# Kernel optimization log

Hardware: AMD Instinct MI355X
Metric: run time of the kernel (lower is better)

Reference implementation:

```python
import jax, jax.numpy as jnp
import numpy as np

NW = 30000      # num_words (word nodes)
ND = 8192       # num_docs
D = 300         # hidden_dim
D2 = D // 2
NNZ_A = 600000  # nnz of word-word adjacency A_norm [NW, NW]
NNZ_X = 524288  # nnz of doc-word tfidf X [ND, NW]
ALPHA = 0.7     # residual_alpha
LN_EPS = 1e-5
BN_SCALE = float(1.0 / np.sqrt(1.0 + 1e-5))  # eval BN, running_mean=0, running_var=1


def _xavier(k, shape):
    fan_out, fan_in = shape[0], shape[1]
    lim = float(np.sqrt(6.0 / (fan_in + fan_out)))
    return jax.random.uniform(k, shape, jnp.float32, -lim, lim)


def setup_inputs() -> dict:
    key = jax.random.key(0)
    ks = jax.random.split(key, 13)
    return {
        "a_rows": jax.random.randint(ks[0], (NNZ_A,), 0, NW, dtype=jnp.int32),
        "a_cols": jax.random.randint(ks[1], (NNZ_A,), 0, NW, dtype=jnp.int32),
        "a_vals": jax.random.uniform(ks[2], (NNZ_A,), jnp.float32) * 0.05,
        "x_rows": jax.random.randint(ks[3], (NNZ_X,), 0, ND, dtype=jnp.int32),
        "x_cols": jax.random.randint(ks[4], (NNZ_X,), 0, NW, dtype=jnp.int32),
        "x_vals": jax.random.uniform(ks[5], (NNZ_X,), jnp.float32) * 0.05,
        "emb": _xavier(ks[6], (NW, D)),
        "w1": _xavier(ks[7], (D, D)),
        "w2": _xavier(ks[8], (D, D)),
        "w3": _xavier(ks[9], (D, D)),
        "ln_g": jnp.ones((D,), jnp.float32),
        "ln_b": jnp.zeros((D,), jnp.float32),
        "m_w1": _xavier(ks[10], (D, D)),
        "m_b1": jnp.zeros((D,), jnp.float32),
        "bn1_g": jnp.ones((D,), jnp.float32),
        "bn1_b": jnp.zeros((D,), jnp.float32),
        "m_w2": _xavier(ks[11], (D2, D)),
        "m_b2": jnp.zeros((D2,), jnp.float32),
        "bn2_g": jnp.ones((D2,), jnp.float32),
        "bn2_b": jnp.zeros((D2,), jnp.float32),
        "clf_w": _xavier(ks[12], (2, D2)),
        "clf_b": jnp.zeros((2,), jnp.float32),
    }


def _spmm(rows, cols, vals, H, n):
    # sparse [n, m] @ dense [m, d] via gather + segment-sum (COO SpMM)
    return jax.ops.segment_sum(vals[:, None] * H[cols], rows, num_segments=n)


def _layernorm(x, g, b):
    mu = jnp.mean(x, axis=-1, keepdims=True)
    var = jnp.var(x, axis=-1, keepdims=True)
    return (x - mu) * jax.lax.rsqrt(var + LN_EPS) * g + b


def _bn_eval(x, g, b):
    # BatchNorm1d in eval mode with freshly-initialized running stats (mean=0, var=1)
    return x * (g * BN_SCALE) + b


def reference(a_rows, a_cols, a_vals, x_rows, x_cols, x_vals, emb, w1, w2, w3,
              ln_g, ln_b, m_w1, m_b1, bn1_g, bn1_b, m_w2, m_b2, bn2_g, bn2_b,
              clf_w, clf_b):
    H0 = emb
    H = jax.nn.relu(_spmm(a_rows, a_cols, a_vals, H0, NW) @ w1.T)
    H = jax.nn.relu(_spmm(a_rows, a_cols, a_vals, H, NW) @ w2.T)
    H = jax.nn.relu(_spmm(a_rows, a_cols, a_vals, H, NW) @ w3.T)
    H = (1.0 - ALPHA) * H0 + ALPHA * H
    word_H = _layernorm(H, ln_g, ln_b)
    # --- doc aggregation: X_tfidf @ word_H + X_tfidf @ emb ---
    doc_H = (_spmm(x_rows, x_cols, x_vals, word_H, ND)
             + _spmm(x_rows, x_cols, x_vals, emb, ND))
    # --- MLP head (dropout inactive in eval) ---
    h = jax.nn.relu(_bn_eval(doc_H @ m_w1.T + m_b1, bn1_g, bn1_b))
    h = jax.nn.relu(_bn_eval(h @ m_w2.T + m_b2, bn2_g, bn2_b))
    return h @ clf_w.T + clf_b  # [ND, 2]
```

## Files before the change

### kernel.cpp

```cpp
#include <hip/hip_runtime.h>

#define NW 30000
#define ND 8192
#define DIM 300
#define DIM2 150
#define NNZA 600000
#define NNZX 524288
#define PD 320
#define PD_U 160
#define BN_SCALE 0.99999500003749971f

typedef unsigned int uint;
typedef unsigned short ushort;
typedef __attribute__((ext_vector_type(8))) short bf16x8;
typedef __attribute__((ext_vector_type(4))) float f32x4;
typedef __attribute__((ext_vector_type(4))) uint uint4v;

static inline int cdiv(int a, int b){ return (a + b - 1) / b; }

__device__ __forceinline__ float b2f_lo(uint u){ return __builtin_bit_cast(float, u << 16); }
__device__ __forceinline__ float b2f_hi(uint u){ return __builtin_bit_cast(float, u & 0xffff0000u); }
__device__ __forceinline__ ushort f2b(float f){
  uint u = __builtin_bit_cast(uint, f);
  u += 0x7fffu + ((u >> 16) & 1u);
  return (ushort)(u >> 16);
}
__device__ __forceinline__ uint packb(float x, float y){
  return (uint)f2b(x) | ((uint)f2b(y) << 16);
}

__global__ void k_hist(const int* __restrict__ rows, int n, int* __restrict__ cnt){
  int i = blockIdx.x * blockDim.x + threadIdx.x;
  if (i < n) atomicAdd(&cnt[rows[i]], 1);
}

__global__ __launch_bounds__(1024) void k_bsum(const int* __restrict__ cnt, int n, int* __restrict__ bs){
  __shared__ int sd[1024];
  int t = threadIdx.x;
  int i = blockIdx.x * 1024 + t;
  sd[t] = (i < n) ? cnt[i] : 0;
  __syncthreads();
  #pragma unroll
  for (int o = 512; o > 0; o >>= 1){
    if (t < o) sd[t] += sd[t + o];
    __syncthreads();
  }
  if (t == 0) bs[blockIdx.x] = sd[0];
}

__global__ __launch_bounds__(64) void k_scan_small(int* __restrict__ bs, int nb,
                                                   int* __restrict__ rp, int n){
  int t = threadIdx.x;
  int orig = (t < nb) ? bs[t] : 0;
  int v = orig;
  #pragma unroll
  for (int o = 1; o < 64; o <<= 1){
    int x = __shfl_up(v, o);
    if (t >= o) v += x;
  }
  if (t < nb) bs[t] = v - orig;
  if (t == nb - 1) rp[n] = v;
}

__global__ __launch_bounds__(1024) void k_scan_apply(const int* __restrict__ cnt, int n,
        const int* __restrict__ bs, int* __restrict__ rp, int* __restrict__ cursor){
  __shared__ int sd[1024];
  int t = threadIdx.x;
  int i = blockIdx.x * 1024 + t;
  int v = (i < n) ? cnt[i] : 0;
  sd[t] = v;
  __syncthreads();
  for (int o = 1; o < 1024; o <<= 1){
    int x = (t >= o) ? sd[t - o] : 0;
    __syncthreads();
    sd[t] += x;
    __syncthreads();
  }
  if (i < n){
    int start = bs[blockIdx.x] + sd[t] - v;
    rp[i] = start;
    cursor[i] = start;
  }
}

__global__ void k_scatter(const int* __restrict__ rows, const int* __restrict__ cols,
                          const float* __restrict__ vals, int n, int* __restrict__ cursor,
                          int* __restrict__ cs, float* __restrict__ vs){
  int i = blockIdx.x * blockDim.x + threadIdx.x;
  if (i < n){
    int r = rows[i];
    int p = atomicAdd(&cursor[r], 1);
    cs[p] = cols[i];
    vs[p] = vals[i];
  }
}

__global__ void k_f2b_pad8(const float* __restrict__ src, ushort* __restrict__ dst,
                           int srows, int scols, int drows, int dstride){
  int q = blockIdx.x * blockDim.x + threadIdx.x;
  int perRow = dstride >> 3;
  int r = q / perRow;
  int c = (q - r * perRow) << 3;
  if (r >= drows) return;
  float x[8];
  #pragma unroll
  for (int j = 0; j < 8; ++j)
    x[j] = (r < srows && c + j < scols) ? src[(size_t)r * scols + c + j] : 0.f;
  uint4v o;
  o.x = packb(x[0], x[1]); o.y = packb(x[2], x[3]);
  o.z = packb(x[4], x[5]); o.w = packb(x[6], x[7]);
  *(uint4v*)(dst + (size_t)r * dstride + c) = o;
}

__global__ void k_f2b_w5(const float* __restrict__ w1, const float* __restrict__ w2,
                         const float* __restrict__ w3, const float* __restrict__ mw1,
                         const float* __restrict__ mw2,
                         ushort* __restrict__ d1, ushort* __restrict__ d2,
                         ushort* __restrict__ d3, ushort* __restrict__ d4,
                         ushort* __restrict__ d5){
  int q = blockIdx.x * blockDim.x + threadIdx.x;
  int r = q / 40;
  int c = (q - r * 40) << 3;
  if (r >= PD) return;
  const float* src; ushort* dst; int srows;
  int wsel = blockIdx.y;
  if      (wsel == 0){ src = w1;  dst = d1; srows = DIM;  }
  else if (wsel == 1){ src = w2;  dst = d2; srows = DIM;  }
  else if (wsel == 2){ src = w3;  dst = d3; srows = DIM;  }
  else if (wsel == 3){ src = mw1; dst = d4; srows = DIM;  }
  else               { src = mw2; dst = d5; srows = DIM2; }
  float x[8];
  #pragma unroll
  for (int j = 0; j < 8; ++j)
    x[j] = (r < srows && c + j < DIM) ? src[(size_t)r * DIM + c + j] : 0.f;
  uint4v o;
  o.x = packb(x[0], x[1]); o.y = packb(x[2], x[3]);
  o.z = packb(x[4], x[5]); o.w = packb(x[6], x[7]);
  *(uint4v*)(dst + (size_t)r * PD + c) = o;
}

__global__ __launch_bounds__(256) void k_spmm_b(const int* __restrict__ rp, const int* __restrict__ cs,
        const float* __restrict__ vs, const uint* __restrict__ Hb, uint* __restrict__ Ob, int nrows){
  int wid = (blockIdx.x * blockDim.x + threadIdx.x) >> 6;
  int lane = threadIdx.x & 63;
  if (wid >= nrows) return;
  int s = rp[wid], e = rp[wid + 1];
  const bool half = lane < 32;
  float acc[4][6] = {};
  int k = s;
  for (; k + 4 <= e; k += 4){
    #pragma unroll
    for (int j = 0; j < 4; ++j){
      int c = cs[k + j];
      float v = vs[k + j];
      const uint* p = Hb + (size_t)c * PD_U;
      uint u0 = p[lane], u1 = p[lane + 64];
      uint u2 = half ? p[lane + 128] : 0;
      acc[j][0] = fmaf(v, b2f_lo(u0), acc[j][0]);
      acc[j][1] = fmaf(v, b2f_hi(u0), acc[j][1]);
      acc[j][2] = fmaf(v, b2f_lo(u1), acc[j][2]);
      acc[j][3] = fmaf(v, b2f_hi(u1), acc[j][3]);
      acc[j][4] = fmaf(v, b2f_lo(u2), acc[j][4]);
      acc[j][5] = fmaf(v, b2f_hi(u2), acc[j][5]);
    }
  }
  for (; k < e; ++k){
    int c = cs[k];
    float v = vs[k];
    const uint* p = Hb + (size_t)c * PD_U;
    uint u0 = p[lane], u1 = p[lane + 64];
    uint u2 = half ? p[lane + 128] : 0;
    acc[0][0] = fmaf(v, b2f_lo(u0), acc[0][0]);
    acc[0][1] = fmaf(v, b2f_hi(u0), acc[0][1]);
    acc[0][2] = fmaf(v, b2f_lo(u1), acc[0][2]);
    acc[0][3] = fmaf(v, b2f_hi(u1), acc[0][3]);
    acc[0][4] = fmaf(v, b2f_lo(u2), acc[0][4]);
    acc[0][5] = fmaf(v, b2f_hi(u2), acc[0][5]);
  }
  #pragma unroll
  for (int d = 0; d < 6; ++d)
    acc[0][d] += (acc[1][d] + acc[2][d]) + acc[3][d];
  uint* o = Ob + (size_t)wid * PD_U;
  o[lane] = packb(acc[0][0], acc[0][1]);
  o[lane + 64] = packb(acc[0][2], acc[0][3]);
  if (half) o[lane + 128] = packb(acc[0][4], acc[0][5]);
}

__global__ __launch_bounds__(256) void k_mgemm(const ushort* __restrict__ A, const ushort* __restrict__ B,
        const float* __restrict__ bias, const float* __restrict__ bng, const float* __restrict__ bnb,
        ushort* __restrict__ C, int M, int Nvalid, int ldc, int relu){
  __shared__ ushort As[128][72];
  __shared__ ushort Bs[160][72];
  const int t = threadIdx.x;
  const int wid = t >> 6, lane = t & 63;
  const int bm = blockIdx.y << 7;
  const int bn = blockIdx.x * 160;
  const int wm = (wid >> 1) << 6;
  const int wn = (wid & 1) * 80;
  const int r16 = lane & 15;
  const int h8 = (lane >> 4) << 3;
  f32x4 acc[4][5] = {};
  for (int k0 = 0; k0 < PD; k0 += 64){
    #pragma unroll
    for (int i = 0; i < 4; ++i){
      int q = t + (i << 8);
      int r = q >> 3, c = (q & 7) << 3;
      int gm = bm + r; if (gm >= M) gm = M - 1;
      *(bf16x8*)(&As[r][c]) = *(const bf16x8*)(A + (size_t)gm * PD + k0 + c);
    }
    #pragma unroll
    for (int i = 0; i < 5; ++i){
      int q = t + (i << 8);
      int r = q >> 3, c = (q & 7) << 3;
      *(bf16x8*)(&Bs[r][c]) = *(const bf16x8*)(B + (size_t)(bn + r) * PD + k0 + c);
    }
    __syncthreads();
    #pragma unroll
    for (int kk = 0; kk < 2; ++kk){
      bf16x8 af[4], bfr[5];
      #pragma unroll
      for (int m = 0; m < 4; ++m)
        af[m] = *(const bf16x8*)(&As[wm + m * 16 + r16][kk * 32 + h8]);
      #pragma unroll
      for (int n = 0; n < 5; ++n)
        bfr[n] = *(const bf16x8*)(&Bs[wn + n * 16 + r16][kk * 32 + h8]);
      #pragma unroll
      for (int m = 0; m < 4; ++m)
        #pragma unroll
        for (int n = 0; n < 5; ++n)
          acc[m][n] = __builtin_amdgcn_mfma_f32_16x16x32_bf16(af[m], bfr[n], acc[m][n], 0, 0, 0);
    }
    __syncthreads();
  }
  const int cr = (lane >> 4) << 2;
  #pragma unroll
  for (int m = 0; m < 4; ++m){
    #pragma unroll
    for (int n = 0; n < 5; ++n){
      int col = bn + wn + n * 16 + r16;
      #pragma unroll
      for (int j = 0; j < 4; ++j){
        int row = bm + wm + m * 16 + cr + j;
        if (row >= M) continue;
        float v = acc[m][n][j];
        if (col < Nvalid){
          if (bias) v += bias[col];
          if (bng)  v = v * (bng[col] * BN_SCALE) + bnb[col];
          if (relu) v = fmaxf(v, 0.f);
        } else v = 0.f;
        C[(size_t)row * ldc + col] = f2b(v);
      }
    }
  }
}

__global__ __launch_bounds__(256) void k_res_ln(const float* __restrict__ emb, const uint* __restrict__ Hb,
        const float* __restrict__ g, const float* __restrict__ bb, uint* __restrict__ S){
  int row = blockIdx.x * 4 + (threadIdx.x >> 6);
  int lane = threadIdx.x & 63;
  if (row >= NW) return;
  const float* e = emb + (size_t)row * DIM;
  const uint* h = Hb + (size_t)row * PD_U;
  float x[6], ev[6];
  float sum = 0.f, sq = 0.f;
  #pragma unroll
  for (int j = 0; j < 3; ++j){
    int i = lane + j * 64;
    float e0 = 0.f, e1 = 0.f, h0 = 0.f, h1 = 0.f;
    if (i < 150){
      uint u = h[i];
      h0 = b2f_lo(u); h1 = b2f_hi(u);
      e0 = e[2 * i]; e1 = e[2 * i + 1];
    }
    float v0 = 0.3f * e0 + 0.7f * h0;
    float v1 = 0.3f * e1 + 0.7f * h1;
    if (i >= 150){ v0 = 0.f; v1 = 0.f; }
    x[2*j] = v0; x[2*j+1] = v1; ev[2*j] = e0; ev[2*j+1] = e1;
    sum += v0 + v1; sq += v0 * v0 + v1 * v1;
  }
  #pragma unroll
  for (int o = 32; o > 0; o >>= 1){ sum += __shfl_down(sum, o); sq += __shfl_down(sq, o); }
  sum = __shfl(sum, 0); sq = __shfl(sq, 0);
  const float inv = 1.f / (float)DIM;
  float mu = sum * inv;
  float var = sq * inv - mu * mu;
  float rs = rsqrtf(var + 1e-5f);
  uint* o = S + (size_t)row * PD_U;
  #pragma unroll
  for (int j = 0; j < 3; ++j){
    int i = lane + j * 64;
    if (i >= PD_U) continue;
    uint w = 0;
    if (i < 150){
      float r0 = (x[2*j]   - mu) * rs * g[2*i]   + bb[2*i]   + ev[2*j];
      float r1 = (x[2*j+1] - mu) * rs * g[2*i+1] + bb[2*i+1] + ev[2*j+1];
      w = packb(r0, r1);
    }
    o[i] = w;
  }
}

__global__ void k_clf(const uint* __restrict__ h2, const float* __restrict__ w,
                      const float* __restrict__ bias, float* __restrict__ out){
  int m = blockIdx.x * blockDim.x + threadIdx.x;
  if (m >= ND) return;
  const uint* hr = h2 + (size_t)m * 80;
  float s0 = bias[0], s1 = bias[1];
  #pragma unroll 5
  for (int i = 0; i < 75; ++i){
    uint u = hr[i];
    float h0 = b2f_lo(u), h1 = b2f_hi(u);
    int k = 2 * i;
    s0 = fmaf(h0, w[k], fmaf(h1, w[k + 1], s0));
    s1 = fmaf(h0, w[DIM2 + k], fmaf(h1, w[DIM2 + k + 1], s1));
  }
  out[m * 2] = s0;
  out[m * 2 + 1] = s1;
}

extern "C" void kernel_launch(void* const* d_in, const int* in_sizes, int n_in,
                              void* d_out, int out_size, void* d_ws, size_t ws_size,
                              hipStream_t stream){
  const int*   a_rows = (const int*)  d_in[0];
  const int*   a_cols = (const int*)  d_in[1];
  const float* a_vals = (const float*)d_in[2];
  const int*   x_rows = (const int*)  d_in[3];
  const int*   x_cols = (const int*)  d_in[4];
  const float* x_vals = (const float*)d_in[5];
  const float* emb    = (const float*)d_in[6];
  const float* w1     = (const float*)d_in[7];
  const float* w2     = (const float*)d_in[8];
  const float* w3     = (const float*)d_in[9];
  const float* ln_g   = (const float*)d_in[10];
  const float* ln_b   = (const float*)d_in[11];
  const float* m_w1   = (const float*)d_in[12];
  const float* m_b1   = (const float*)d_in[13];
  const float* bn1_g  = (const float*)d_in[14];
  const float* bn1_b  = (const float*)d_in[15];
  const float* m_w2   = (const float*)d_in[16];
  const float* m_b2   = (const float*)d_in[17];
  const float* bn2_g  = (const float*)d_in[18];
  const float* bn2_b  = (const float*)d_in[19];
  const float* clf_w  = (const float*)d_in[20];
  const float* clf_b  = (const float*)d_in[21];
  float* out = (float*)d_out;

  char* ws = (char*)d_ws;
  size_t off = 0;
  auto take = [&](size_t nbytes)->void*{
    void* p = ws + off;
    off += (nbytes + 255) & ~(size_t)255;
    return p;
  };
  int*    a_rp   = (int*)   take((NW + 1) * 4);
  int*    a_cs   = (int*)   take((size_t)NNZA * 4);
  float*  a_vs   = (float*) take((size_t)NNZA * 4);
  int*    x_rp   = (int*)   take((ND + 1) * 4);
  int*    x_cs   = (int*)   take((size_t)NNZX * 4);
  float*  x_vs   = (float*) take((size_t)NNZX * 4);
  int*    cursor = (int*)   take((size_t)NW * 4);
  int*    bsums  = (int*)   take(64 * 4);
  ushort* embb   = (ushort*)take((size_t)NW * PD * 2);
  ushort* Tb     = (ushort*)take((size_t)NW * PD * 2);
  ushort* Hb     = (ushort*)take((size_t)NW * PD * 2);
  ushort* w1b    = (ushort*)take((size_t)PD * PD * 2);
  ushort* w2b    = (ushort*)take((size_t)PD * PD * 2);
  ushort* w3b    = (ushort*)take((size_t)PD * PD * 2);
  ushort* mw1b   = (ushort*)take((size_t)PD * PD * 2);
  ushort* mw2b   = (ushort*)take((size_t)PD * PD * 2);
  ushort* docHb = Hb;
  ushort* h1b   = Hb + (size_t)ND * PD;
  ushort* h2b   = Hb + (size_t)2 * ND * PD;

  int nbA = cdiv(NW, 1024);
  hipMemsetAsync(cursor, 0, NW * 4, stream);
  k_hist<<<cdiv(NNZA, 256), 256, 0, stream>>>(a_rows, NNZA, cursor);
  k_bsum<<<nbA, 1024, 0, stream>>>(cursor, NW, bsums);
  k_scan_small<<<1, 64, 0, stream>>>(bsums, nbA, a_rp, NW);
  k_scan_apply<<<nbA, 1024, 0, stream>>>(cursor, NW, bsums, a_rp, cursor);
  k_scatter<<<cdiv(NNZA, 256), 256, 0, stream>>>(a_rows, a_cols, a_vals, NNZA, cursor, a_cs, a_vs);
  int nbX = cdiv(ND, 1024);
  hipMemsetAsync(cursor, 0, ND * 4, stream);
  k_hist<<<cdiv(NNZX, 256), 256, 0, stream>>>(x_rows, NNZX, cursor);
  k_bsum<<<nbX, 1024, 0, stream>>>(cursor, ND, bsums);
  k_scan_small<<<1, 64, 0, stream>>>(bsums, nbX, x_rp, ND);
  k_scan_apply<<<nbX, 1024, 0, stream>>>(cursor, ND, bsums, x_rp, cursor);
  k_scatter<<<cdiv(NNZX, 256), 256, 0, stream>>>(x_rows, x_cols, x_vals, NNZX, cursor, x_cs, x_vs);

  k_f2b_pad8<<<cdiv(NW * 40, 256), 256, 0, stream>>>(emb, embb, NW, DIM, NW, PD);
  dim3 gw(cdiv(PD * 40, 256), 5);
  k_f2b_w5<<<gw, 256, 0, stream>>>(w1, w2, w3, m_w1, m_w2, w1b, w2b, w3b, mw1b, mw2b);

  dim3 gg(2, cdiv(NW, 128));
  k_spmm_b<<<cdiv(NW, 4), 256, 0, stream>>>(a_rp, a_cs, a_vs, (const uint*)embb, (uint*)Tb, NW);
  k_mgemm<<<gg, 256, 0, stream>>>(Tb, w1b, nullptr, nullptr, nullptr, Hb, NW, DIM, PD, 1);
  k_spmm_b<<<cdiv(NW, 4), 256, 0, stream>>>(a_rp, a_cs, a_vs, (const uint*)Hb, (uint*)Tb, NW);
  k_mgemm<<<gg, 256, 0, stream>>>(Tb, w2b, nullptr, nullptr, nullptr, Hb, NW, DIM, PD, 1);
  k_spmm_b<<<cdiv(NW, 4), 256, 0, stream>>>(a_rp, a_cs, a_vs, (const uint*)Hb, (uint*)Tb, NW);
  k_mgemm<<<gg, 256, 0, stream>>>(Tb, w3b, nullptr, nullptr, nullptr, Hb, NW, DIM, PD, 1);
  k_res_ln<<<cdiv(NW, 4), 256, 0, stream>>>(emb, (const uint*)Hb, ln_g, ln_b, (uint*)Tb);
  k_spmm_b<<<cdiv(ND, 4), 256, 0, stream>>>(x_rp, x_cs, x_vs, (const uint*)Tb, (uint*)docHb, ND);
  dim3 g1(2, cdiv(ND, 128));
  k_mgemm<<<g1, 256, 0, stream>>>(docHb, mw1b, m_b1, bn1_g, bn1_b, h1b, ND, DIM, PD, 1);
  dim3 g2(1, cdiv(ND, 128));
  k_mgemm<<<g2, 256, 0, stream>>>(h1b, mw2b, m_b2, bn2_g, bn2_b, h2b, ND, DIM2, 160, 1);
  k_clf<<<cdiv(ND, 256), 256, 0, stream>>>((const uint*)h2b, clf_w, clf_b, out);
}
```

Baseline: 539.5 us.

## Merge CSR build and conversion launches, read bf16 emb in LN, warp-parallel classifier

Batches the A and X CSR construction (histogram, block sums, scan, scatter) and the emb/weight bf16 conversions into a few multi-purpose kernels selected by blockIdx.y. This cuts the launch count from about 14 to 5. The residual LayerNorm now reads the bf16-packed embedding instead of fp32 emb, which reduces its memory traffic but uses a rounded residual term. The classifier moves from one thread per row to one wavefront per row with shuffle reductions, for coalesced loads.

```diff
diff --git a/kernel.cpp b/kernel.cpp
--- a/kernel.cpp
+++ b/kernel.cpp
@@ -8,6 +8,8 @@
 #define NNZX 524288
 #define PD 320
 #define PD_U 160
+#define NBA 30
+#define NBX 8
 #define BN_SCALE 0.99999500003749971f
 
 typedef unsigned int uint;
@@ -29,13 +31,22 @@
   return (uint)f2b(x) | ((uint)f2b(y) << 16);
 }
 
-__global__ void k_hist(const int* __restrict__ rows, int n, int* __restrict__ cnt){
+__global__ void k_hist2(const int* __restrict__ ra, const int* __restrict__ rx,
+                        int* __restrict__ cntA, int* __restrict__ cntX){
   int i = blockIdx.x * blockDim.x + threadIdx.x;
-  if (i < n) atomicAdd(&cnt[rows[i]], 1);
-}
-
-__global__ __launch_bounds__(1024) void k_bsum(const int* __restrict__ cnt, int n, int* __restrict__ bs){
+  if (blockIdx.y == 0){
+    if (i < NNZA) atomicAdd(&cntA[ra[i]], 1);
+  } else {
+    if (i < NNZX) atomicAdd(&cntX[rx[i]], 1);
+  }
+}
+
+__global__ __launch_bounds__(1024) void k_bsum2(const int* __restrict__ cntA, const int* __restrict__ cntX,
+                                                int* __restrict__ bsA, int* __restrict__ bsX){
   __shared__ int sd[1024];
+  const int* cnt; int n; int* bs;
+  if (blockIdx.y == 0){ cnt = cntA; n = NW; bs = bsA; }
+  else                { cnt = cntX; n = ND; bs = bsX; }
   int t = threadIdx.x;
   int i = blockIdx.x * 1024 + t;
   sd[t] = (i < n) ? cnt[i] : 0;
@@ -48,23 +59,32 @@
   if (t == 0) bs[blockIdx.x] = sd[0];
 }
 
-__global__ __launch_bounds__(64) void k_scan_small(int* __restrict__ bs, int nb,
-                                                   int* __restrict__ rp, int n){
-  int t = threadIdx.x;
-  int orig = (t < nb) ? bs[t] : 0;
+__global__ __launch_bounds__(128) void k_scan_small2(int* __restrict__ bsA, int* __restrict__ bsX,
+                                                     int* __restrict__ a_rp, int* __restrict__ x_rp){
+  int w = threadIdx.x >> 6, lane = threadIdx.x & 63;
+  int* bs = w ? bsX : bsA;
+  int nb  = w ? NBX : NBA;
+  int* rp = w ? x_rp : a_rp;
+  int n   = w ? ND : NW;
+  int orig = (lane < nb) ? bs[lane] : 0;
   int v = orig;
   #pragma unroll
   for (int o = 1; o < 64; o <<= 1){
     int x = __shfl_up(v, o);
-    if (t >= o) v += x;
-  }
-  if (t < nb) bs[t] = v - orig;
-  if (t == nb - 1) rp[n] = v;
-}
-
-__global__ __launch_bounds__(1024) void k_scan_apply(const int* __restrict__ cnt, int n,
-        const int* __restrict__ bs, int* __restrict__ rp, int* __restrict__ cursor){
+    if (lane >= o) v += x;
+  }
+  if (lane < nb) bs[lane] = v - orig;
+  if (lane == nb - 1) rp[n] = v;
+}
+
+__global__ __launch_bounds__(1024) void k_scan_apply2(const int* __restrict__ cntA, const int* __restrict__ cntX,
+        const int* __restrict__ bsA, const int* __restrict__ bsX,
+        int* __restrict__ a_rp, int* __restrict__ x_rp,
+        int* __restrict__ curA, int* __restrict__ curX){
   __shared__ int sd[1024];
+  const int* cnt; const int* bs; int n; int* rp; int* cur;
+  if (blockIdx.y == 0){ cnt = cntA; bs = bsA; n = NW; rp = a_rp; cur = curA; }
+  else                { cnt = cntX; bs = bsX; n = ND; rp = x_rp; cur = curX; }
   int t = threadIdx.x;
   int i = blockIdx.x * 1024 + t;
   int v = (i < n) ? cnt[i] : 0;
@@ -79,64 +99,69 @@
   if (i < n){
     int start = bs[blockIdx.x] + sd[t] - v;
     rp[i] = start;
-    cursor[i] = start;
-  }
-}
-
-__global__ void k_scatter(const int* __restrict__ rows, const int* __restrict__ cols,
-                          const float* __restrict__ vals, int n, int* __restrict__ cursor,
-                          int* __restrict__ cs, float* __restrict__ vs){
-  int i = blockIdx.x * blockDim.x + threadIdx.x;
-  if (i < n){
-    int r = rows[i];
-    int p = atomicAdd(&cursor[r], 1);
-    cs[p] = cols[i];
-    vs[p] = vals[i];
-  }
-}
-
-__global__ void k_f2b_pad8(const float* __restrict__ src, ushort* __restrict__ dst,
-                           int srows, int scols, int drows, int dstride){
-  int q = blockIdx.x * blockDim.x + threadIdx.x;
-  int perRow = dstride >> 3;
-  int r = q / perRow;
-  int c = (q - r * perRow) << 3;
-  if (r >= drows) return;
-  float x[8];
-  #pragma unroll
-  for (int j = 0; j < 8; ++j)
-    x[j] = (r < srows && c + j < scols) ? src[(size_t)r * scols + c + j] : 0.f;
-  uint4v o;
-  o.x = packb(x[0], x[1]); o.y = packb(x[2], x[3]);
-  o.z = packb(x[4], x[5]); o.w = packb(x[6], x[7]);
-  *(uint4v*)(dst + (size_t)r * dstride + c) = o;
-}
-
-__global__ void k_f2b_w5(const float* __restrict__ w1, const float* __restrict__ w2,
-                         const float* __restrict__ w3, const float* __restrict__ mw1,
-                         const float* __restrict__ mw2,
-                         ushort* __restrict__ d1, ushort* __restrict__ d2,
-                         ushort* __restrict__ d3, ushort* __restrict__ d4,
-                         ushort* __restrict__ d5){
-  int q = blockIdx.x * blockDim.x + threadIdx.x;
-  int r = q / 40;
-  int c = (q - r * 40) << 3;
-  if (r >= PD) return;
-  const float* src; ushort* dst; int srows;
-  int wsel = blockIdx.y;
-  if      (wsel == 0){ src = w1;  dst = d1; srows = DIM;  }
-  else if (wsel == 1){ src = w2;  dst = d2; srows = DIM;  }
-  else if (wsel == 2){ src = w3;  dst = d3; srows = DIM;  }
-  else if (wsel == 3){ src = mw1; dst = d4; srows = DIM;  }
-  else               { src = mw2; dst = d5; srows = DIM2; }
-  float x[8];
-  #pragma unroll
-  for (int j = 0; j < 8; ++j)
-    x[j] = (r < srows && c + j < DIM) ? src[(size_t)r * DIM + c + j] : 0.f;
-  uint4v o;
-  o.x = packb(x[0], x[1]); o.y = packb(x[2], x[3]);
-  o.z = packb(x[4], x[5]); o.w = packb(x[6], x[7]);
-  *(uint4v*)(dst + (size_t)r * PD + c) = o;
+    cur[i] = start;
+  }
+}
+
+__global__ void k_prep(const int* __restrict__ a_rows, const int* __restrict__ a_cols, const float* __restrict__ a_vals,
+                       const int* __restrict__ x_rows, const int* __restrict__ x_cols, const float* __restrict__ x_vals,
+                       int* __restrict__ curA, int* __restrict__ curX,
+                       int* __restrict__ a_cs, float* __restrict__ a_vs,
+                       int* __restrict__ x_cs, float* __restrict__ x_vs,
+                       const float* __restrict__ emb, ushort* __restrict__ embb,
+                       const float* __restrict__ w1, const float* __restrict__ w2, const float* __restrict__ w3,
+                       const float* __restrict__ mw1, const float* __restrict__ mw2,
+                       ushort* __restrict__ w1b, ushort* __restrict__ w2b, ushort* __restrict__ w3b,
+                       ushort* __restrict__ mw1b, ushort* __restrict__ mw2b){
+  int y = blockIdx.y;
+  int gi = blockIdx.x * blockDim.x + threadIdx.x;
+  if (y == 0){
+    if (gi < NNZA){
+      int r = a_rows[gi];
+      int p = atomicAdd(&curA[r], 1);
+      a_cs[p] = a_cols[gi];
+      a_vs[p] = a_vals[gi];
+    }
+  } else if (y == 1){
+    if (gi < NNZX){
+      int r = x_rows[gi];
+      int p = atomicAdd(&curX[r], 1);
+      x_cs[p] = x_cols[gi];
+      x_vs[p] = x_vals[gi];
+    }
+  } else if (y == 2){
+    if (gi < NW * 40){
+      int r = gi / 40;
+      int c = (gi - r * 40) << 3;
+      float x[8];
+      #pragma unroll
+      for (int j = 0; j < 8; ++j)
+        x[j] = (c + j < DIM) ? emb[(size_t)r * DIM + c + j] : 0.f;
+      uint4v o;
+      o.x = packb(x[0], x[1]); o.y = packb(x[2], x[3]);
+      o.z = packb(x[4], x[5]); o.w = packb(x[6], x[7]);
+      *(uint4v*)(embb + (size_t)r * PD + c) = o;
+    }
+  } else {
+    if (gi < PD * 40){
+      int r = gi / 40;
+      int c = (gi - r * 40) << 3;
+      const float* src; ushort* dst; int srows;
+      if      (y == 3){ src = w1;  dst = w1b;  srows = DIM;  }
+      else if (y == 4){ src = w2;  dst = w2b;  srows = DIM;  }
+      else if (y == 5){ src = w3;  dst = w3b;  srows = DIM;  }
+      else if (y == 6){ src = mw1; dst = mw1b; srows = DIM;  }
+      else            { src = mw2; dst = mw2b; srows = DIM2; }
+      float x[8];
+      #pragma unroll
+      for (int j = 0; j < 8; ++j)
+        x[j] = (r < srows && c + j < DIM) ? src[(size_t)r * DIM + c + j] : 0.f;
+      uint4v o;
+      o.x = packb(x[0], x[1]); o.y = packb(x[2], x[3]);
+      o.z = packb(x[4], x[5]); o.w = packb(x[6], x[7]);
+      *(uint4v*)(dst + (size_t)r * PD + c) = o;
+    }
+  }
 }
 
 __global__ __launch_bounds__(256) void k_spmm_b(const int* __restrict__ rp, const int* __restrict__ cs,
@@ -254,12 +279,12 @@
   }
 }
 
-__global__ __launch_bounds__(256) void k_res_ln(const float* __restrict__ emb, const uint* __restrict__ Hb,
+__global__ __launch_bounds__(256) void k_res_ln(const uint* __restrict__ E, const uint* __restrict__ Hb,
         const float* __restrict__ g, const float* __restrict__ bb, uint* __restrict__ S){
   int row = blockIdx.x * 4 + (threadIdx.x >> 6);
   int lane = threadIdx.x & 63;
   if (row >= NW) return;
-  const float* e = emb + (size_t)row * DIM;
+  const uint* e = E + (size_t)row * PD_U;
   const uint* h = Hb + (size_t)row * PD_U;
   float x[6], ev[6];
   float sum = 0.f, sq = 0.f;
@@ -269,8 +294,9 @@
     float e0 = 0.f, e1 = 0.f, h0 = 0.f, h1 = 0.f;
     if (i < 150){
       uint u = h[i];
-      h0 = b2f_lo(u); h1 = b2f_hi(u);
-      e0 = e[2 * i]; e1 = e[2 * i + 1];
+      uint ue = e[i];
+      h0 = b2f_lo(u);  h1 = b2f_hi(u);
+      e0 = b2f_lo(ue); e1 = b2f_hi(ue);
     }
     float v0 = 0.3f * e0 + 0.7f * h0;
     float v1 = 0.3f * e1 + 0.7f * h1;
@@ -300,22 +326,35 @@
   }
 }
 
-__global__ void k_clf(const uint* __restrict__ h2, const float* __restrict__ w,
+__global__ __launch_bounds__(256) void k_clf(const uint* __restrict__ h2, const float* __restrict__ w,
                       const float* __restrict__ bias, float* __restrict__ out){
-  int m = blockIdx.x * blockDim.x + threadIdx.x;
-  if (m >= ND) return;
-  const uint* hr = h2 + (size_t)m * 80;
-  float s0 = bias[0], s1 = bias[1];
-  #pragma unroll 5
-  for (int i = 0; i < 75; ++i){
-    uint u = hr[i];
+  int row = blockIdx.x * 4 + (threadIdx.x >> 6);
+  int lane = threadIdx.x & 63;
+  if (row >= ND) return;
+  float s0, s1;
+  {
+    uint u = h2[(size_t)row * 80 + lane];
     float h0 = b2f_lo(u), h1 = b2f_hi(u);
-    int k = 2 * i;
-    s0 = fmaf(h0, w[k], fmaf(h1, w[k + 1], s0));
-    s1 = fmaf(h0, w[DIM2 + k], fmaf(h1, w[DIM2 + k + 1], s1));
-  }
-  out[m * 2] = s0;
-  out[m * 2 + 1] = s1;
+    int k = 2 * lane;
+    s0 = h0 * w[k] + h1 * w[k + 1];
+    s1 = h0 * w[DIM2 + k] + h1 * w[DIM2 + k + 1];
+  }
+  if (lane < 11){
+    uint u = h2[(size_t)row * 80 + 64 + lane];
+    float h0 = b2f_lo(u), h1 = b2f_hi(u);
+    int k = 2 * (64 + lane);
+    s0 += h0 * w[k] + h1 * w[k + 1];
+    s1 += h0 * w[DIM2 + k] + h1 * w[DIM2 + k + 1];
+  }
+  #pragma unroll
+  for (int o = 32; o > 0; o >>= 1){
+    s0 += __shfl_down(s0, o);
+    s1 += __shfl_down(s1, o);
+  }
+  if (lane == 0){
+    out[row * 2]     = s0 + bias[0];
+    out[row * 2 + 1] = s1 + bias[1];
+  }
 }
 
 extern "C" void kernel_launch(void* const* d_in, const int* in_sizes, int n_in,
@@ -358,8 +397,9 @@
   int*    x_rp   = (int*)   take((ND + 1) * 4);
   int*    x_cs   = (int*)   take((size_t)NNZX * 4);
   float*  x_vs   = (float*) take((size_t)NNZX * 4);
-  int*    cursor = (int*)   take((size_t)NW * 4);
-  int*    bsums  = (int*)   take(64 * 4);
+  int*    cursors= (int*)   take((size_t)(NW + ND) * 4);
+  int*    bsA    = (int*)   take(64 * 4);
+  int*    bsX    = (int*)   take(64 * 4);
   ushort* embb   = (ushort*)take((size_t)NW * PD * 2);
   ushort* Tb     = (ushort*)take((size_t)NW * PD * 2);
   ushort* Hb     = (ushort*)take((size_t)NW * PD * 2);
@@ -368,28 +408,24 @@
   ushort* w3b    = (ushort*)take((size_t)PD * PD * 2);
   ushort* mw1b   = (ushort*)take((size_t)PD * PD * 2);
   ushort* mw2b   = (ushort*)take((size_t)PD * PD * 2);
+  int* curA = cursors;
+  int* curX = cursors + NW;
   ushort* docHb = Hb;
   ushort* h1b   = Hb + (size_t)ND * PD;
   ushort* h2b   = Hb + (size_t)2 * ND * PD;
 
-  int nbA = cdiv(NW, 1024);
-  hipMemsetAsync(cursor, 0, NW * 4, stream);
-  k_hist<<<cdiv(NNZA, 256), 256, 0, stream>>>(a_rows, NNZA, cursor);
-  k_bsum<<<nbA, 1024, 0, stream>>>(cursor, NW, bsums);
-  k_scan_small<<<1, 64, 0, stream>>>(bsums, nbA, a_rp, NW);
-  k_scan_apply<<<nbA, 1024, 0, stream>>>(cursor, NW, bsums, a_rp, cursor);
-  k_scatter<<<cdiv(NNZA, 256), 256, 0, stream>>>(a_rows, a_cols, a_vals, NNZA, cursor, a_cs, a_vs);
-  int nbX = cdiv(ND, 1024);
-  hipMemsetAsync(cursor, 0, ND * 4, stream);
-  k_hist<<<cdiv(NNZX, 256), 256, 0, stream>>>(x_rows, NNZX, cursor);
-  k_bsum<<<nbX, 1024, 0, stream>>>(cursor, ND, bsums);
-  k_scan_small<<<1, 64, 0, stream>>>(bsums, nbX, x_rp, ND);
-  k_scan_apply<<<nbX, 1024, 0, stream>>>(cursor, ND, bsums, x_rp, cursor);
-  k_scatter<<<cdiv(NNZX, 256), 256, 0, stream>>>(x_rows, x_cols, x_vals, NNZX, cursor, x_cs, x_vs);
-
-  k_f2b_pad8<<<cdiv(NW * 40, 256), 256, 0, stream>>>(emb, embb, NW, DIM, NW, PD);
-  dim3 gw(cdiv(PD * 40, 256), 5);
-  k_f2b_w5<<<gw, 256, 0, stream>>>(w1, w2, w3, m_w1, m_w2, w1b, w2b, w3b, mw1b, mw2b);
+  hipMemsetAsync(cursors, 0, (size_t)(NW + ND) * 4, stream);
+  dim3 gh(cdiv(NNZA, 256), 2);
+  k_hist2<<<gh, 256, 0, stream>>>(a_rows, x_rows, curA, curX);
+  dim3 gb(NBA, 2);
+  k_bsum2<<<gb, 1024, 0, stream>>>(curA, curX, bsA, bsX);
+  k_scan_small2<<<1, 128, 0, stream>>>(bsA, bsX, a_rp, x_rp);
+  k_scan_apply2<<<gb, 1024, 0, stream>>>(curA, curX, bsA, bsX, a_rp, x_rp, curA, curX);
+  dim3 gp(cdiv(NW * 40, 256), 8);
+  k_prep<<<gp, 256, 0, stream>>>(a_rows, a_cols, a_vals, x_rows, x_cols, x_vals,
+                                 curA, curX, a_cs, a_vs, x_cs, x_vs,
+                                 emb, embb, w1, w2, w3, m_w1, m_w2,
+                                 w1b, w2b, w3b, mw1b, mw2b);
 
   dim3 gg(2, cdiv(NW, 128));
   k_spmm_b<<<cdiv(NW, 4), 256, 0, stream>>>(a_rp, a_cs, a_vs, (const uint*)embb, (uint*)Tb, NW);
@@ -398,11 +434,11 @@
   k_mgemm<<<gg, 256, 0, stream>>>(Tb, w2b, nullptr, nullptr, nullptr, Hb, NW, DIM, PD, 1);
   k_spmm_b<<<cdiv(NW, 4), 256, 0, stream>>>(a_rp, a_cs, a_vs, (const uint*)Hb, (uint*)Tb, NW);
   k_mgemm<<<gg, 256, 0, stream>>>(Tb, w3b, nullptr, nullptr, nullptr, Hb, NW, DIM, PD, 1);
-  k_res_ln<<<cdiv(NW, 4), 256, 0, stream>>>(emb, (const uint*)Hb, ln_g, ln_b, (uint*)Tb);
+  k_res_ln<<<cdiv(NW, 4), 256, 0, stream>>>((const uint*)embb, (const uint*)Hb, ln_g, ln_b, (uint*)Tb);
   k_spmm_b<<<cdiv(ND, 4), 256, 0, stream>>>(x_rp, x_cs, x_vs, (const uint*)Tb, (uint*)docHb, ND);
   dim3 g1(2, cdiv(ND, 128));
   k_mgemm<<<g1, 256, 0, stream>>>(docHb, mw1b, m_b1, bn1_g, bn1_b, h1b, ND, DIM, PD, 1);
   dim3 g2(1, cdiv(ND, 128));
   k_mgemm<<<g2, 256, 0, stream>>>(h1b, mw2b, m_b2, bn2_g, bn2_b, h2b, ND, DIM2, 160, 1);
-  k_clf<<<cdiv(ND, 256), 256, 0, stream>>>((const uint*)h2b, clf_w, clf_b, out);
-}
+  k_clf<<<cdiv(ND, 4), 256, 0, stream>>>((const uint*)h2b, clf_w, clf_b, out);
+}
```

After: 507.0 us. -6.0%, faster.
